# Optimization experiments

Hardware: AMD Instinct MI355X
Metric: run time of the kernel (lower is better)

The kernel has to match this reference:

```python
import jax, jax.numpy as jnp
import numpy as np
import math

D_MODEL = 512
N_TOTAL = 1024
HW = 4096
EPSILON = 0.2
NUM_HEADS = 8
D_K = D_MODEL // NUM_HEADS
BATCH = 4


def setup_inputs() -> dict:
    rng = jax.random.key(0)
    ks = jax.random.split(rng, 16)
    s = 1.0 / math.sqrt(D_MODEL)
    inp = {
        "query": jax.random.normal(ks[0], (BATCH, N_TOTAL, D_MODEL), jnp.float32),
        "key": jax.random.normal(ks[1], (BATCH, HW, D_MODEL), jnp.float32),
        "value": jax.random.normal(ks[2], (BATCH, HW, D_MODEL), jnp.float32),
        "x_tilde": jax.random.uniform(ks[3], (HW, 2), jnp.float32),
        "x_hat": jax.random.uniform(ks[4], (N_TOTAL, HW, 2), jnp.float32),
        # torch nn.Linear params: W is (out, in), y = x @ W.T + b
        "Wq": jax.random.uniform(ks[5], (D_MODEL, D_MODEL), jnp.float32, -s, s),
        "bq": jax.random.uniform(ks[6], (D_MODEL,), jnp.float32, -s, s),
        "Wk": jax.random.uniform(ks[7], (D_MODEL, D_MODEL), jnp.float32, -s, s),
        "bk": jax.random.uniform(ks[8], (D_MODEL,), jnp.float32, -s, s),
        "Wv": jax.random.uniform(ks[9], (D_MODEL, D_MODEL), jnp.float32, -s, s),
        "bv": jax.random.uniform(ks[10], (D_MODEL,), jnp.float32, -s, s),
        "Wo": jax.random.uniform(ks[11], (D_MODEL, D_MODEL), jnp.float32, -s, s),
        "bo": jax.random.uniform(ks[12], (D_MODEL,), jnp.float32, -s, s),
    }
    return inp


def _geo_mask(x_tilde, x_hat):
    # x_tilde: (HW, 2), x_hat: (N_total, HW, 2)
    diff = x_tilde[None, :, :] - x_hat            # (N, HW, 2)
    dist = jnp.sqrt(jnp.sum(diff * diff, axis=-1))  # (N, HW)
    return jnp.where(dist < EPSILON, 0.0, -jnp.inf).astype(x_hat.dtype)


def reference(query, key, value, x_tilde, x_hat, Wq, bq, Wk, bk, Wv, bv, Wo, bo):
    B = query.shape[0]
    M_geo = _geo_mask(x_tilde, x_hat)  # (N, HW)

    def heads(x, W, b):
        y = x @ W.T + b                                   # (B, L, D)
        return y.reshape(B, -1, NUM_HEADS, D_K).transpose(0, 2, 1, 3)  # (B, H, L, dk)

    Q = heads(query, Wq, bq)   # (B, H, N, dk)
    K = heads(key, Wk, bk)     # (B, H, HW, dk)
    V = heads(value, Wv, bv)   # (B, H, HW, dk)

    scores = jnp.einsum("bhnd,bhmd->bhnm", Q, K) / math.sqrt(D_K)
    scores = scores + M_geo[None, None, :, :]
    attn = jax.nn.softmax(scores, axis=-1)                # (B, H, N, HW)
    ctx = jnp.einsum("bhnm,bhmd->bhnd", attn, V)          # (B, H, N, dk)
    ctx = ctx.transpose(0, 2, 1, 3).reshape(B, -1, D_MODEL)
    out = ctx @ Wo.T + bo                                 # (B, N, D)
    return out, attn
```

## Files before the change

kernel.cpp:

```cpp
#include <hip/hip_runtime.h>
#include <cstdint>
#include <cstddef>

typedef __attribute__((ext_vector_type(4))) float f32x4;
typedef __attribute__((ext_vector_type(8))) short s16x8;
typedef __attribute__((ext_vector_type(4))) short s16x4;
typedef unsigned short u16;
typedef unsigned long long u64;

static __device__ inline u16 f2bf(float f) {
    unsigned u = __builtin_bit_cast(unsigned, f);
    u += 0x7fffu + ((u >> 16) & 1u);
    return (u16)(u >> 16);
}

static __device__ inline f32x4 mfma16(s16x8 a, s16x8 b, f32x4 c) {
    return __builtin_amdgcn_mfma_f32_16x16x32_bf16(a, b, c, 0, 0, 0);
}

static __device__ inline float redmax16(float v) {
    v = fmaxf(v, __shfl_xor(v, 1));
    v = fmaxf(v, __shfl_xor(v, 2));
    v = fmaxf(v, __shfl_xor(v, 4));
    v = fmaxf(v, __shfl_xor(v, 8));
    return v;
}
static __device__ inline float redsum16(float v) {
    v += __shfl_xor(v, 1);
    v += __shfl_xor(v, 2);
    v += __shfl_xor(v, 4);
    v += __shfl_xor(v, 8);
    return v;
}

__global__ __launch_bounds__(256) void cvt_bf16_kernel(const float* __restrict__ src,
                                                       u16* __restrict__ dst, float scale) {
    int i = (blockIdx.x * 256 + threadIdx.x) * 4;
    f32x4 v = *(const f32x4*)(src + i);
    s16x4 o;
    o[0] = (short)f2bf(v[0] * scale); o[1] = (short)f2bf(v[1] * scale);
    o[2] = (short)f2bf(v[2] * scale); o[3] = (short)f2bf(v[3] * scale);
    *(s16x4*)(dst + i) = o;
}

__global__ __launch_bounds__(256) void mask_kernel(const float* __restrict__ xt,
                                                   const float* __restrict__ xh,
                                                   u64* __restrict__ mb) {
    int tid  = threadIdx.x;
    int lane = tid & 63;
    int wv   = blockIdx.x * 4 + (tid >> 6);
    int n    = wv >> 6;
    int mbk  = wv & 63;
    int m    = (mbk << 6) + lane;
    size_t hidx = ((size_t)n * 4096 + m) * 2;
    float dx = xt[2 * m]     - xh[hidx];
    float dy = xt[2 * m + 1] - xh[hidx + 1];
    bool p = sqrtf(dx * dx + dy * dy) < 0.2f;
    u64 bal = __ballot(p);
    if (lane == 0) mb[wv] = bal;
}

template <int INF32, int MODE, int LSHIFT>
__global__ __launch_bounds__(256) void proj_kernel(const void* __restrict__ Xv,
                                                   const u16* __restrict__ Wb,
                                                   const float* __restrict__ bias,
                                                   float bscale,
                                                   void* __restrict__ Yv) {
    __shared__ u16 aT[64 * 72];
    __shared__ u16 bT[64 * 72];

    int tid  = threadIdx.x;
    int lane = tid & 63, w = tid >> 6, q = lane >> 4, m15 = lane & 15;
    int m0 = blockIdx.x * 64, n0 = blockIdx.y * 64;
    int rT = tid >> 2, cT = tid & 3;

    f32x4 cacc[4];
#pragma unroll
    for (int i = 0; i < 4; ++i) { f32x4 z = {0.f, 0.f, 0.f, 0.f}; cacc[i] = z; }

    for (int kb = 0; kb < 512; kb += 64) {
        if (INF32) {
            const float* X = (const float*)Xv;
#pragma unroll
            for (int j = 0; j < 4; ++j) {
                int k = cT * 4 + j * 16;
                f32x4 v = *(const f32x4*)(X + (size_t)(m0 + rT) * 512 + kb + k);
                s16x4 o;
                o[0] = (short)f2bf(v[0]); o[1] = (short)f2bf(v[1]);
                o[2] = (short)f2bf(v[2]); o[3] = (short)f2bf(v[3]);
                *(s16x4*)(aT + rT * 72 + k) = o;
            }
        } else {
            const u16* X = (const u16*)Xv;
#pragma unroll
            for (int j = 0; j < 2; ++j) {
                int k = cT * 8 + j * 32;
                s16x8 v = *(const s16x8*)(X + (size_t)(m0 + rT) * 512 + kb + k);
                *(s16x8*)(aT + rT * 72 + k) = v;
            }
        }
#pragma unroll
        for (int j = 0; j < 2; ++j) {
            int k = cT * 8 + j * 32;
            s16x8 v = *(const s16x8*)(Wb + (size_t)(n0 + rT) * 512 + kb + k);
            *(s16x8*)(bT + rT * 72 + k) = v;
        }
        __syncthreads();
#pragma unroll
        for (int kk = 0; kk < 2; ++kk) {
            s16x8 af = *(const s16x8*)(aT + (w * 16 + m15) * 72 + kk * 32 + q * 8);
#pragma unroll
            for (int nt = 0; nt < 4; ++nt) {
                s16x8 bf = *(const s16x8*)(bT + (nt * 16 + m15) * 72 + kk * 32 + q * 8);
                cacc[nt] = mfma16(af, bf, cacc[nt]);
            }
        }
        __syncthreads();
    }

#pragma unroll
    for (int nt = 0; nt < 4; ++nt) {
        int col = n0 + nt * 16 + m15;
        float bv = bias[col] * bscale;
        int mbase = m0 + w * 16 + q * 4;
        if (MODE == 2) {
            float* Y = (float*)Yv;
#pragma unroll
            for (int r = 0; r < 4; ++r)
                Y[(size_t)(mbase + r) * 512 + col] = cacc[nt][r] + bv;
        } else if (MODE == 3) {
            u16* Y = (u16*)Yv;
            int hh = col >> 6, d = col & 63;
#pragma unroll
            for (int r = 0; r < 4; ++r) {
                int mg = mbase + r;
                int bb = mg >> LSHIFT;
                int nn = mg & ((1 << LSHIFT) - 1);
                Y[(((size_t)(bb * 8 + hh) << LSHIFT) + nn) * 64 + d] = f2bf(cacc[nt][r] + bv);
            }
        } else {
            u16* Yt = (u16*)Yv;
            int bidx = mbase >> 12, hw0 = mbase & 4095;
            int hh = col >> 6, d = col & 63;
            s16x4 o;
#pragma unroll
            for (int r = 0; r < 4; ++r) o[r] = (short)f2bf(cacc[nt][r] + bv);
            *(s16x4*)(Yt + ((size_t)((bidx << 3) + hh) * 64 + d) * 4096 + hw0) = o;
        }
    }
}

__global__ __launch_bounds__(512) void attn_kernel(const u16* __restrict__ Qh,
                                                   const u16* __restrict__ Kh,
                                                   const u16* __restrict__ Vt,
                                                   const u64* __restrict__ mbits,
                                                   float* __restrict__ attnO,
                                                   u16* __restrict__ ctxO) {
    __shared__ float sred[8][16];
    __shared__ float srowm[16];
    __shared__ float srowi[16];
    __shared__ u16   sps[8][2][640];
    __shared__ float sctx[1024];

    int tid  = threadIdx.x;
    int lane = tid & 63, w = tid >> 6, q = lane >> 4, m15 = lane & 15;
    int i = blockIdx.x;
    int bh = (i & 7) + ((i >> 3) & 3) * 8;
    int n0 = (i >> 5) * 16;
    int b = bh >> 3, h = bh & 7;

    for (int j = tid; j < 1024; j += 512) sctx[j] = 0.f;

    const u16* Qp = Qh + (((size_t)bh << 10) + n0 + m15) * 64 + q * 8;
    s16x8 aQ0 = *(const s16x8*)(Qp);
    s16x8 aQ1 = *(const s16x8*)(Qp + 32);

    const u16* Kp = Kh + (((size_t)bh << 12) + (w << 9) + m15) * 64 + q * 8;
    f32x4 acc[32];
#pragma unroll
    for (int t = 0; t < 32; ++t) {
        const u16* kp = Kp + (size_t)t * (16 * 64);
        s16x8 b0 = *(const s16x8*)(kp);
        s16x8 b1 = *(const s16x8*)(kp + 32);
        f32x4 c = {0.f, 0.f, 0.f, 0.f};
        c = mfma16(aQ0, b0, c);
        c = mfma16(aQ1, b1, c);
        acc[t] = c;
    }

    const float NEGINF = -__builtin_huge_valf();
    float mr[4] = {NEGINF, NEGINF, NEGINF, NEGINF};
    const u64* mrow = mbits + (size_t)n0 * 64;
#pragma unroll
    for (int t4 = 0; t4 < 8; ++t4) {
        int widx = (w << 3) + t4;
        u64 mk[4];
#pragma unroll
        for (int r = 0; r < 4; ++r) mk[r] = mrow[(q * 4 + r) * 64 + widx];
#pragma unroll
        for (int tt = 0; tt < 4; ++tt) {
            int t = t4 * 4 + tt;
            int bit = tt * 16 + m15;
#pragma unroll
            for (int r = 0; r < 4; ++r) {
                float s = acc[t][r];
                s = ((mk[r] >> bit) & 1ull) ? s : NEGINF;
                acc[t][r] = s;
                mr[r] = fmaxf(mr[r], s);
            }
        }
    }
#pragma unroll
    for (int r = 0; r < 4; ++r) mr[r] = redmax16(mr[r]);
    if (m15 == 0) {
#pragma unroll
        for (int r = 0; r < 4; ++r) sred[w][q * 4 + r] = mr[r];
    }
    __syncthreads();
    if (tid < 16) {
        float mm = sred[0][tid];
#pragma unroll
        for (int ww = 1; ww < 8; ++ww) mm = fmaxf(mm, sred[ww][tid]);
        srowm[tid] = mm;
    }
    __syncthreads();
    const float L2E = 1.44269504f;
    float bb[4];
#pragma unroll
    for (int r = 0; r < 4; ++r) bb[r] = srowm[q * 4 + r] * L2E;

    float ls[4] = {0.f, 0.f, 0.f, 0.f};
#pragma unroll
    for (int t = 0; t < 32; ++t) {
#pragma unroll
        for (int r = 0; r < 4; ++r) {
            float p = exp2f(__builtin_fmaf(acc[t][r], L2E, -bb[r]));
            acc[t][r] = p;
            ls[r] += p;
        }
    }
#pragma unroll
    for (int r = 0; r < 4; ++r) ls[r] = redsum16(ls[r]);
    if (m15 == 0) {
#pragma unroll
        for (int r = 0; r < 4; ++r) sred[w][q * 4 + r] = ls[r];
    }
    __syncthreads();
    if (tid < 16) {
        float ss = 0.f;
#pragma unroll
        for (int ww = 0; ww < 8; ++ww) ss += sred[ww][tid];
        srowi[tid] = 1.0f / ss;
    }
    __syncthreads();
    float iv[4];
#pragma unroll
    for (int r = 0; r < 4; ++r) iv[r] = srowi[q * 4 + r];

    const u16* Vp = Vt + (((size_t)bh << 6) + m15) * 4096 + (w << 9) + q * 8;
    const u16* psr0 = &sps[w][0][m15 * 40 + q * 8];
    const u16* psr1 = &sps[w][1][m15 * 40 + q * 8];

    f32x4 ctxa[4];
#pragma unroll
    for (int j = 0; j < 4; ++j) { f32x4 z = {0.f, 0.f, 0.f, 0.f}; ctxa[j] = z; }

#pragma unroll
    for (int cc = 0; cc < 16; ++cc) {
        u16* pw = &sps[w][cc & 1][0];
#pragma unroll
        for (int sub = 0; sub < 2; ++sub) {
            int t = cc * 2 + sub;
#pragma unroll
            for (int r = 0; r < 4; ++r)
                pw[(q * 4 + r) * 40 + sub * 16 + m15] = f2bf(acc[t][r]);
        }
        s16x8 aP = *(const s16x8*)((cc & 1) ? psr1 : psr0);
#pragma unroll
        for (int dt = 0; dt < 4; ++dt) {
            s16x8 bV = *(const s16x8*)(Vp + dt * (16 * 4096) + cc * 32);
            ctxa[dt] = mfma16(aP, bV, ctxa[dt]);
        }
    }

    float* aB = attnO + (((size_t)bh << 10) + n0 + q * 4) * 4096 + (w << 9) + m15;
#pragma unroll
    for (int t = 0; t < 32; ++t) {
#pragma unroll
        for (int r = 0; r < 4; ++r)
            __builtin_nontemporal_store(acc[t][r] * iv[r], aB + (size_t)r * 4096 + t * 16);
    }

#pragma unroll
    for (int dt = 0; dt < 4; ++dt)
#pragma unroll
        for (int r = 0; r < 4; ++r)
            atomicAdd(&sctx[(q * 4 + r) * 64 + dt * 16 + m15], ctxa[dt][r] * iv[r]);
    __syncthreads();
    for (int j = tid; j < 1024; j += 512) {
        int rr = j >> 6, d = j & 63;
        ctxO[(((size_t)b << 10) + n0 + rr) * 512 + h * 64 + d] = f2bf(sctx[j]);
    }
}

extern "C" void kernel_launch(void* const* d_in, const int* in_sizes, int n_in,
                              void* d_out, int out_size, void* d_ws, size_t ws_size,
                              hipStream_t stream) {
    (void)in_sizes; (void)n_in; (void)out_size; (void)ws_size;
    const float* query = (const float*)d_in[0];
    const float* key   = (const float*)d_in[1];
    const float* value = (const float*)d_in[2];
    const float* x_tilde = (const float*)d_in[3];
    const float* x_hat   = (const float*)d_in[4];
    const float* Wq = (const float*)d_in[5];  const float* bq = (const float*)d_in[6];
    const float* Wk = (const float*)d_in[7];  const float* bk = (const float*)d_in[8];
    const float* Wv = (const float*)d_in[9];  const float* bv = (const float*)d_in[10];
    const float* Wo = (const float*)d_in[11]; const float* bo = (const float*)d_in[12];

    char* ws = (char*)d_ws;
    u16* wq   = (u16*)(ws + 0);
    u16* wk   = (u16*)(ws + 524288);
    u16* wv   = (u16*)(ws + 1048576);
    u16* wo   = (u16*)(ws + 1572864);
    u16* Qh   = (u16*)(ws + 2097152);
    u16* Kh   = (u16*)(ws + 6291456);
    u16* Vtb  = (u16*)(ws + 23068672);
    u16* ctxb = (u16*)(ws + 39845888);
    u64* mbits = (u64*)(ws + 44040192);

    cvt_bf16_kernel<<<256, 256, 0, stream>>>(Wq, wq, 0.125f);
    cvt_bf16_kernel<<<256, 256, 0, stream>>>(Wk, wk, 1.0f);
    cvt_bf16_kernel<<<256, 256, 0, stream>>>(Wv, wv, 1.0f);
    cvt_bf16_kernel<<<256, 256, 0, stream>>>(Wo, wo, 1.0f);
    mask_kernel<<<16384, 256, 0, stream>>>(x_tilde, x_hat, mbits);

    proj_kernel<1, 3, 10><<<dim3(64, 8),  256, 0, stream>>>(query, wq, bq, 0.125f, Qh);
    proj_kernel<1, 3, 12><<<dim3(256, 8), 256, 0, stream>>>(key,   wk, bk, 1.0f,   Kh);
    proj_kernel<1, 1, 12><<<dim3(256, 8), 256, 0, stream>>>(value, wv, bv, 1.0f,   Vtb);

    float* attnO = (float*)d_out + 2097152;
    attn_kernel<<<2048, 512, 0, stream>>>(Qh, Kh, Vtb, mbits, attnO, ctxb);

    proj_kernel<0, 2, 10><<<dim3(64, 8), 256, 0, stream>>>(ctxb, wo, bo, 1.0f, d_out);
}
```

Baseline: 998.8 us.

## Enlarge projection GEMM tiles and restructure attention into two-pass recompute without max

The projection GEMM tile grows from 64x64 to 128x128 with a 2x2 warp layout and a 4x4 MFMA accumulator grid per warp, which raises operand reuse. The attention kernel now handles 32 query rows per block, stages the mask bits in LDS, and drops the row-max pass. A first pass sums exp(score), and a second pass recomputes QK^T to write normalized probabilities and accumulate P·V. This removes the 32-tile register-resident score array and one reduction pass, at the cost of computing QK^T twice. Without max subtraction, exp of large scores could overflow, and the attention output stores are no longer nontemporal.

Result: faster. 921.6 us (-7.7%).

```diff
diff --git a/kernel.cpp b/kernel.cpp
--- a/kernel.cpp
+++ b/kernel.cpp
@@ -18,13 +18,6 @@
     return __builtin_amdgcn_mfma_f32_16x16x32_bf16(a, b, c, 0, 0, 0);
 }
 
-static __device__ inline float redmax16(float v) {
-    v = fmaxf(v, __shfl_xor(v, 1));
-    v = fmaxf(v, __shfl_xor(v, 2));
-    v = fmaxf(v, __shfl_xor(v, 4));
-    v = fmaxf(v, __shfl_xor(v, 8));
-    return v;
-}
 static __device__ inline float redsum16(float v) {
     v += __shfl_xor(v, 1);
     v += __shfl_xor(v, 2);
@@ -66,86 +59,97 @@
                                                    const float* __restrict__ bias,
                                                    float bscale,
                                                    void* __restrict__ Yv) {
-    __shared__ u16 aT[64 * 72];
-    __shared__ u16 bT[64 * 72];
+    __shared__ u16 aT[128 * 72];
+    __shared__ u16 bT[128 * 72];
 
     int tid  = threadIdx.x;
     int lane = tid & 63, w = tid >> 6, q = lane >> 4, m15 = lane & 15;
-    int m0 = blockIdx.x * 64, n0 = blockIdx.y * 64;
-    int rT = tid >> 2, cT = tid & 3;
-
-    f32x4 cacc[4];
-#pragma unroll
-    for (int i = 0; i < 4; ++i) { f32x4 z = {0.f, 0.f, 0.f, 0.f}; cacc[i] = z; }
+    int wm = w >> 1, wn = w & 1;
+    int m0 = blockIdx.x * 128, n0 = blockIdx.y * 128;
+    int sRow = tid >> 1, sC = (tid & 1) * 32;
+
+    f32x4 acc[4][4];
+#pragma unroll
+    for (int i = 0; i < 4; ++i)
+#pragma unroll
+        for (int j = 0; j < 4; ++j) { f32x4 z = {0.f, 0.f, 0.f, 0.f}; acc[i][j] = z; }
 
     for (int kb = 0; kb < 512; kb += 64) {
         if (INF32) {
             const float* X = (const float*)Xv;
 #pragma unroll
-            for (int j = 0; j < 4; ++j) {
-                int k = cT * 4 + j * 16;
-                f32x4 v = *(const f32x4*)(X + (size_t)(m0 + rT) * 512 + kb + k);
+            for (int j = 0; j < 8; ++j) {
+                int col = sC + j * 4;
+                f32x4 v = *(const f32x4*)(X + (size_t)(m0 + sRow) * 512 + kb + col);
                 s16x4 o;
                 o[0] = (short)f2bf(v[0]); o[1] = (short)f2bf(v[1]);
                 o[2] = (short)f2bf(v[2]); o[3] = (short)f2bf(v[3]);
-                *(s16x4*)(aT + rT * 72 + k) = o;
+                *(s16x4*)(aT + sRow * 72 + col) = o;
             }
         } else {
             const u16* X = (const u16*)Xv;
 #pragma unroll
-            for (int j = 0; j < 2; ++j) {
-                int k = cT * 8 + j * 32;
-                s16x8 v = *(const s16x8*)(X + (size_t)(m0 + rT) * 512 + kb + k);
-                *(s16x8*)(aT + rT * 72 + k) = v;
-            }
-        }
-#pragma unroll
-        for (int j = 0; j < 2; ++j) {
-            int k = cT * 8 + j * 32;
-            s16x8 v = *(const s16x8*)(Wb + (size_t)(n0 + rT) * 512 + kb + k);
-            *(s16x8*)(bT + rT * 72 + k) = v;
+            for (int j = 0; j < 4; ++j) {
+                int col = sC + j * 8;
+                s16x8 v = *(const s16x8*)(X + (size_t)(m0 + sRow) * 512 + kb + col);
+                *(s16x8*)(aT + sRow * 72 + col) = v;
+            }
+        }
+#pragma unroll
+        for (int j = 0; j < 4; ++j) {
+            int col = sC + j * 8;
+            s16x8 v = *(const s16x8*)(Wb + (size_t)(n0 + sRow) * 512 + kb + col);
+            *(s16x8*)(bT + sRow * 72 + col) = v;
         }
         __syncthreads();
 #pragma unroll
         for (int kk = 0; kk < 2; ++kk) {
-            s16x8 af = *(const s16x8*)(aT + (w * 16 + m15) * 72 + kk * 32 + q * 8);
-#pragma unroll
-            for (int nt = 0; nt < 4; ++nt) {
-                s16x8 bf = *(const s16x8*)(bT + (nt * 16 + m15) * 72 + kk * 32 + q * 8);
-                cacc[nt] = mfma16(af, bf, cacc[nt]);
-            }
+            s16x8 af[4], bf[4];
+#pragma unroll
+            for (int t = 0; t < 4; ++t) {
+                af[t] = *(const s16x8*)(aT + (wm * 64 + t * 16 + m15) * 72 + kk * 32 + q * 8);
+                bf[t] = *(const s16x8*)(bT + (wn * 64 + t * 16 + m15) * 72 + kk * 32 + q * 8);
+            }
+#pragma unroll
+            for (int am = 0; am < 4; ++am)
+#pragma unroll
+                for (int bn = 0; bn < 4; ++bn)
+                    acc[am][bn] = mfma16(af[am], bf[bn], acc[am][bn]);
         }
         __syncthreads();
     }
 
 #pragma unroll
-    for (int nt = 0; nt < 4; ++nt) {
-        int col = n0 + nt * 16 + m15;
-        float bv = bias[col] * bscale;
-        int mbase = m0 + w * 16 + q * 4;
-        if (MODE == 2) {
-            float* Y = (float*)Yv;
-#pragma unroll
-            for (int r = 0; r < 4; ++r)
-                Y[(size_t)(mbase + r) * 512 + col] = cacc[nt][r] + bv;
-        } else if (MODE == 3) {
-            u16* Y = (u16*)Yv;
-            int hh = col >> 6, d = col & 63;
-#pragma unroll
-            for (int r = 0; r < 4; ++r) {
-                int mg = mbase + r;
-                int bb = mg >> LSHIFT;
-                int nn = mg & ((1 << LSHIFT) - 1);
-                Y[(((size_t)(bb * 8 + hh) << LSHIFT) + nn) * 64 + d] = f2bf(cacc[nt][r] + bv);
-            }
-        } else {
-            u16* Yt = (u16*)Yv;
-            int bidx = mbase >> 12, hw0 = mbase & 4095;
-            int hh = col >> 6, d = col & 63;
-            s16x4 o;
-#pragma unroll
-            for (int r = 0; r < 4; ++r) o[r] = (short)f2bf(cacc[nt][r] + bv);
-            *(s16x4*)(Yt + ((size_t)((bidx << 3) + hh) * 64 + d) * 4096 + hw0) = o;
+    for (int am = 0; am < 4; ++am) {
+        int mg = m0 + wm * 64 + am * 16 + q * 4;
+#pragma unroll
+        for (int bn = 0; bn < 4; ++bn) {
+            int col = n0 + wn * 64 + bn * 16 + m15;
+            float bv = bias[col] * bscale;
+            if (MODE == 2) {
+                float* Y = (float*)Yv;
+#pragma unroll
+                for (int r = 0; r < 4; ++r)
+                    Y[(size_t)(mg + r) * 512 + col] = acc[am][bn][r] + bv;
+            } else if (MODE == 3) {
+                u16* Y = (u16*)Yv;
+                int hh = col >> 6, d = col & 63;
+#pragma unroll
+                for (int r = 0; r < 4; ++r) {
+                    int m = mg + r;
+                    int bb = m >> LSHIFT;
+                    int nn = m & ((1 << LSHIFT) - 1);
+                    Y[(((size_t)(bb * 8 + hh) << LSHIFT) + nn) * 64 + d] = f2bf(acc[am][bn][r] + bv);
+                }
+            } else {
+                u16* Yt = (u16*)Yv;
+                int bidx = mg >> 12, hw0 = mg & 4095;
+                int hh = col >> 6, d = col & 63;
+                s16x4 o;
+#pragma unroll
+                for (int r = 0; r < 4; ++r) o[r] = (short)f2bf(acc[am][bn][r] + bv);
+                *(s16x4*)(Yt + ((size_t)((bidx << 3) + hh) * 64 + d) * 4096 + hw0) = o;
+            }
         }
     }
 }
@@ -156,150 +160,156 @@
                                                    const u64* __restrict__ mbits,
                                                    float* __restrict__ attnO,
                                                    u16* __restrict__ ctxO) {
-    __shared__ float sred[8][16];
-    __shared__ float srowm[16];
-    __shared__ float srowi[16];
-    __shared__ u16   sps[8][2][640];
-    __shared__ float sctx[1024];
+    __shared__ u64   smask[2048];
+    __shared__ float sred[8][32];
+    __shared__ float srowi[32];
+    __shared__ u16   sps[8][2][16 * 72];
+    __shared__ float sctx[2048];
 
     int tid  = threadIdx.x;
     int lane = tid & 63, w = tid >> 6, q = lane >> 4, m15 = lane & 15;
     int i = blockIdx.x;
-    int bh = (i & 7) + ((i >> 3) & 3) * 8;
-    int n0 = (i >> 5) * 16;
+    int jj = i >> 3;
+    int bh = (i & 7) * 4 + (jj & 3);
+    int n0 = (jj >> 2) * 32;
     int b = bh >> 3, h = bh & 7;
 
-    for (int j = tid; j < 1024; j += 512) sctx[j] = 0.f;
-
-    const u16* Qp = Qh + (((size_t)bh << 10) + n0 + m15) * 64 + q * 8;
-    s16x8 aQ0 = *(const s16x8*)(Qp);
-    s16x8 aQ1 = *(const s16x8*)(Qp + 32);
+    for (int t = tid; t < 2048; t += 512) {
+        smask[t] = mbits[(size_t)n0 * 64 + t];
+        sctx[t]  = 0.f;
+    }
+    __syncthreads();
+
+    s16x8 aQ[2][2];
+#pragma unroll
+    for (int g = 0; g < 2; ++g) {
+        const u16* Qp = Qh + (((size_t)bh << 10) + n0 + g * 16 + m15) * 64 + q * 8;
+        aQ[g][0] = *(const s16x8*)(Qp);
+        aQ[g][1] = *(const s16x8*)(Qp + 32);
+    }
 
     const u16* Kp = Kh + (((size_t)bh << 12) + (w << 9) + m15) * 64 + q * 8;
-    f32x4 acc[32];
-#pragma unroll
-    for (int t = 0; t < 32; ++t) {
-        const u16* kp = Kp + (size_t)t * (16 * 64);
-        s16x8 b0 = *(const s16x8*)(kp);
-        s16x8 b1 = *(const s16x8*)(kp + 32);
-        f32x4 c = {0.f, 0.f, 0.f, 0.f};
-        c = mfma16(aQ0, b0, c);
-        c = mfma16(aQ1, b1, c);
-        acc[t] = c;
-    }
-
-    const float NEGINF = -__builtin_huge_valf();
-    float mr[4] = {NEGINF, NEGINF, NEGINF, NEGINF};
-    const u64* mrow = mbits + (size_t)n0 * 64;
-#pragma unroll
+    const float L2E = 1.44269504f;
+
+    float ls[2][4] = {{0.f,0.f,0.f,0.f},{0.f,0.f,0.f,0.f}};
     for (int t4 = 0; t4 < 8; ++t4) {
-        int widx = (w << 3) + t4;
-        u64 mk[4];
-#pragma unroll
-        for (int r = 0; r < 4; ++r) mk[r] = mrow[(q * 4 + r) * 64 + widx];
+        int widx = w * 8 + t4;
+        u64 mk[2][4];
+#pragma unroll
+        for (int g = 0; g < 2; ++g)
+#pragma unroll
+            for (int r = 0; r < 4; ++r) mk[g][r] = smask[(g * 16 + q * 4 + r) * 64 + widx];
 #pragma unroll
         for (int tt = 0; tt < 4; ++tt) {
-            int t = t4 * 4 + tt;
+            const u16* kp = Kp + (size_t)(t4 * 4 + tt) * (16 * 64);
+            s16x8 b0 = *(const s16x8*)(kp);
+            s16x8 b1 = *(const s16x8*)(kp + 32);
+            f32x4 z = {0.f, 0.f, 0.f, 0.f};
+            f32x4 c0 = mfma16(aQ[0][0], b0, mfma16(aQ[0][1], b1, z));
+            f32x4 c1 = mfma16(aQ[1][0], b0, mfma16(aQ[1][1], b1, z));
             int bit = tt * 16 + m15;
 #pragma unroll
             for (int r = 0; r < 4; ++r) {
-                float s = acc[t][r];
-                s = ((mk[r] >> bit) & 1ull) ? s : NEGINF;
-                acc[t][r] = s;
-                mr[r] = fmaxf(mr[r], s);
-            }
-        }
-    }
-#pragma unroll
-    for (int r = 0; r < 4; ++r) mr[r] = redmax16(mr[r]);
-    if (m15 == 0) {
-#pragma unroll
-        for (int r = 0; r < 4; ++r) sred[w][q * 4 + r] = mr[r];
-    }
+                float p0 = ((mk[0][r] >> bit) & 1ull) ? exp2f(c0[r] * L2E) : 0.f;
+                float p1 = ((mk[1][r] >> bit) & 1ull) ? exp2f(c1[r] * L2E) : 0.f;
+                ls[0][r] += p0;
+                ls[1][r] += p1;
+            }
+        }
+    }
+#pragma unroll
+    for (int g = 0; g < 2; ++g)
+#pragma unroll
+        for (int r = 0; r < 4; ++r) {
+            float v = redsum16(ls[g][r]);
+            if (m15 == 0) sred[w][g * 16 + q * 4 + r] = v;
+        }
     __syncthreads();
-    if (tid < 16) {
-        float mm = sred[0][tid];
-#pragma unroll
-        for (int ww = 1; ww < 8; ++ww) mm = fmaxf(mm, sred[ww][tid]);
-        srowm[tid] = mm;
-    }
-    __syncthreads();
-    const float L2E = 1.44269504f;
-    float bb[4];
-#pragma unroll
-    for (int r = 0; r < 4; ++r) bb[r] = srowm[q * 4 + r] * L2E;
-
-    float ls[4] = {0.f, 0.f, 0.f, 0.f};
-#pragma unroll
-    for (int t = 0; t < 32; ++t) {
-#pragma unroll
-        for (int r = 0; r < 4; ++r) {
-            float p = exp2f(__builtin_fmaf(acc[t][r], L2E, -bb[r]));
-            acc[t][r] = p;
-            ls[r] += p;
-        }
-    }
-#pragma unroll
-    for (int r = 0; r < 4; ++r) ls[r] = redsum16(ls[r]);
-    if (m15 == 0) {
-#pragma unroll
-        for (int r = 0; r < 4; ++r) sred[w][q * 4 + r] = ls[r];
-    }
-    __syncthreads();
-    if (tid < 16) {
+    if (tid < 32) {
         float ss = 0.f;
 #pragma unroll
         for (int ww = 0; ww < 8; ++ww) ss += sred[ww][tid];
         srowi[tid] = 1.0f / ss;
     }
     __syncthreads();
-    float iv[4];
-#pragma unroll
-    for (int r = 0; r < 4; ++r) iv[r] = srowi[q * 4 + r];
+    float iv[2][4];
+#pragma unroll
+    for (int g = 0; g < 2; ++g)
+#pragma unroll
+        for (int r = 0; r < 4; ++r) iv[g][r] = srowi[g * 16 + q * 4 + r];
 
     const u16* Vp = Vt + (((size_t)bh << 6) + m15) * 4096 + (w << 9) + q * 8;
-    const u16* psr0 = &sps[w][0][m15 * 40 + q * 8];
-    const u16* psr1 = &sps[w][1][m15 * 40 + q * 8];
-
-    f32x4 ctxa[4];
-#pragma unroll
-    for (int j = 0; j < 4; ++j) { f32x4 z = {0.f, 0.f, 0.f, 0.f}; ctxa[j] = z; }
-
-#pragma unroll
-    for (int cc = 0; cc < 16; ++cc) {
-        u16* pw = &sps[w][cc & 1][0];
-#pragma unroll
-        for (int sub = 0; sub < 2; ++sub) {
-            int t = cc * 2 + sub;
+    float* aBp[2];
+#pragma unroll
+    for (int g = 0; g < 2; ++g)
+        aBp[g] = attnO + (((size_t)bh << 10) + n0 + g * 16 + q * 4) * 4096 + (w << 9) + m15;
+
+    f32x4 ctxa[2][4];
+#pragma unroll
+    for (int g = 0; g < 2; ++g)
+#pragma unroll
+        for (int dt = 0; dt < 4; ++dt) { f32x4 z = {0.f, 0.f, 0.f, 0.f}; ctxa[g][dt] = z; }
+
+    for (int cc = 0; cc < 8; ++cc) {
+        int widx = w * 8 + cc;
+        u64 mk[2][4];
+#pragma unroll
+        for (int g = 0; g < 2; ++g)
+#pragma unroll
+            for (int r = 0; r < 4; ++r) mk[g][r] = smask[(g * 16 + q * 4 + r) * 64 + widx];
+
+        f32x4 cs[2][4];
+#pragma unroll
+        for (int tt = 0; tt < 4; ++tt) {
+            const u16* kp = Kp + (size_t)(cc * 4 + tt) * (16 * 64);
+            s16x8 b0 = *(const s16x8*)(kp);
+            s16x8 b1 = *(const s16x8*)(kp + 32);
+            f32x4 z = {0.f, 0.f, 0.f, 0.f};
+            f32x4 c0 = mfma16(aQ[0][0], b0, mfma16(aQ[0][1], b1, z));
+            f32x4 c1 = mfma16(aQ[1][0], b0, mfma16(aQ[1][1], b1, z));
+            int bit = tt * 16 + m15;
+#pragma unroll
+            for (int r = 0; r < 4; ++r) {
+                float p0 = ((mk[0][r] >> bit) & 1ull) ? exp2f(c0[r] * L2E) : 0.f;
+                float p1 = ((mk[1][r] >> bit) & 1ull) ? exp2f(c1[r] * L2E) : 0.f;
+                sps[w][0][(q * 4 + r) * 72 + tt * 16 + m15] = f2bf(p0);
+                sps[w][1][(q * 4 + r) * 72 + tt * 16 + m15] = f2bf(p1);
+                cs[0][tt][r] = p0 * iv[0][r];
+                cs[1][tt][r] = p1 * iv[1][r];
+            }
+        }
+#pragma unroll
+        for (int g = 0; g < 2; ++g)
+#pragma unroll
+            for (int half = 0; half < 2; ++half) {
+                s16x8 aP = *(const s16x8*)(&sps[w][g][m15 * 72 + half * 32 + q * 8]);
+#pragma unroll
+                for (int dt = 0; dt < 4; ++dt) {
+                    s16x8 bV = *(const s16x8*)(Vp + (size_t)dt * (16 * 4096) + cc * 64 + half * 32);
+                    ctxa[g][dt] = mfma16(aP, bV, ctxa[g][dt]);
+                }
+            }
+#pragma unroll
+        for (int g = 0; g < 2; ++g)
+#pragma unroll
+            for (int tt = 0; tt < 4; ++tt)
+#pragma unroll
+                for (int r = 0; r < 4; ++r)
+                    aBp[g][(size_t)r * 4096 + cc * 64 + tt * 16] = cs[g][tt][r];
+    }
+
+#pragma unroll
+    for (int g = 0; g < 2; ++g)
+#pragma unroll
+        for (int dt = 0; dt < 4; ++dt)
 #pragma unroll
             for (int r = 0; r < 4; ++r)
-                pw[(q * 4 + r) * 40 + sub * 16 + m15] = f2bf(acc[t][r]);
-        }
-        s16x8 aP = *(const s16x8*)((cc & 1) ? psr1 : psr0);
-#pragma unroll
-        for (int dt = 0; dt < 4; ++dt) {
-            s16x8 bV = *(const s16x8*)(Vp + dt * (16 * 4096) + cc * 32);
-            ctxa[dt] = mfma16(aP, bV, ctxa[dt]);
-        }
-    }
-
-    float* aB = attnO + (((size_t)bh << 10) + n0 + q * 4) * 4096 + (w << 9) + m15;
-#pragma unroll
-    for (int t = 0; t < 32; ++t) {
-#pragma unroll
-        for (int r = 0; r < 4; ++r)
-            __builtin_nontemporal_store(acc[t][r] * iv[r], aB + (size_t)r * 4096 + t * 16);
-    }
-
-#pragma unroll
-    for (int dt = 0; dt < 4; ++dt)
-#pragma unroll
-        for (int r = 0; r < 4; ++r)
-            atomicAdd(&sctx[(q * 4 + r) * 64 + dt * 16 + m15], ctxa[dt][r] * iv[r]);
+                atomicAdd(&sctx[(g * 16 + q * 4 + r) * 64 + dt * 16 + m15],
+                          ctxa[g][dt][r] * iv[g][r]);
     __syncthreads();
-    for (int j = tid; j < 1024; j += 512) {
-        int rr = j >> 6, d = j & 63;
-        ctxO[(((size_t)b << 10) + n0 + rr) * 512 + h * 64 + d] = f2bf(sctx[j]);
+    for (int t = tid; t < 2048; t += 512) {
+        int rr = t >> 6, d = t & 63;
+        ctxO[(((size_t)b << 10) + n0 + rr) * 512 + h * 64 + d] = f2bf(sctx[t]);
     }
 }
 
@@ -334,12 +344,12 @@
     cvt_bf16_kernel<<<256, 256, 0, stream>>>(Wo, wo, 1.0f);
     mask_kernel<<<16384, 256, 0, stream>>>(x_tilde, x_hat, mbits);
 
-    proj_kernel<1, 3, 10><<<dim3(64, 8),  256, 0, stream>>>(query, wq, bq, 0.125f, Qh);
-    proj_kernel<1, 3, 12><<<dim3(256, 8), 256, 0, stream>>>(key,   wk, bk, 1.0f,   Kh);
-    proj_kernel<1, 1, 12><<<dim3(256, 8), 256, 0, stream>>>(value, wv, bv, 1.0f,   Vtb);
+    proj_kernel<1, 3, 10><<<dim3(32, 4),  256, 0, stream>>>(query, wq, bq, 0.125f, Qh);
+    proj_kernel<1, 3, 12><<<dim3(128, 4), 256, 0, stream>>>(key,   wk, bk, 1.0f,   Kh);
+    proj_kernel<1, 1, 12><<<dim3(128, 4), 256, 0, stream>>>(value, wv, bv, 1.0f,   Vtb);
 
     float* attnO = (float*)d_out + 2097152;
-    attn_kernel<<<2048, 512, 0, stream>>>(Qh, Kh, Vtb, mbits, attnO, ctxb);
-
-    proj_kernel<0, 2, 10><<<dim3(64, 8), 256, 0, stream>>>(ctxb, wo, bo, 1.0f, d_out);
-}
+    attn_kernel<<<1024, 512, 0, stream>>>(Qh, Kh, Vtb, mbits, attnO, ctxb);
+
+    proj_kernel<0, 2, 10><<<dim3(32, 4), 256, 0, stream>>>(ctxb, wo, bo, 1.0f, d_out);
+}
```
